# Performance work log

Hardware: AMD Instinct MI355X
Metric: run time of the kernel (lower is better)

The kernel has to match this reference:

```python
import jax, jax.numpy as jnp
import numpy as np

N, E, H = 50000, 300000, 8  # nodes, edges, FeaStConv heads (PyG default)


def _lin_init(k, fan_in, fan_out):
    k1, k2 = jax.random.split(k)
    s = 1.0 / np.sqrt(fan_in)
    w = jax.random.uniform(k1, (fan_in, fan_out), jnp.float32, -s, s)
    b = jax.random.uniform(k2, (fan_out,), jnp.float32, -s, s)
    return w, b


def _conv_init(k, cin, cout):
    k1, k2 = jax.random.split(k)
    w = jax.random.normal(k1, (cin, H * cout), jnp.float32) * 0.1   # weight
    u = jax.random.normal(k2, (cin, H), jnp.float32) * 0.1          # attention u
    c = jnp.zeros((H,), jnp.float32)                                 # attention bias
    b = jnp.zeros((cout,), jnp.float32)                              # output bias
    return w, u, c, b


def setup_inputs() -> dict:
    key = jax.random.key(0)
    ks = jax.random.split(key, 10)
    x = jax.random.normal(ks[0], (N, 3), jnp.float32)
    src = jax.random.randint(ks[1], (E,), 0, N)
    dst = jax.random.randint(ks[2], (E,), 0, N)
    dst = jnp.where(src == dst, (dst + 1) % N, dst)  # no self loops in raw edge list
    edge_index = jnp.stack([src, dst]).astype(jnp.int64)
    labels = (jax.random.uniform(ks[3], (N, 1)) < 0.1).astype(jnp.float32)
    lin1_w, lin1_b = _lin_init(ks[4], 3, 16)
    c1_w, c1_u, c1_c, c1_b = _conv_init(ks[5], 16, 32)
    c2_w, c2_u, c2_c, c2_b = _conv_init(ks[6], 32, 64)
    c3_w, c3_u, c3_c, c3_b = _conv_init(ks[7], 64, 128)
    lin2_w, lin2_b = _lin_init(ks[8], 128, 1024)
    lin3_w, lin3_b = _lin_init(ks[9], 1024, 1)
    return dict(x=x, edge_index=edge_index, labels=labels,
                lin1_w=lin1_w, lin1_b=lin1_b,
                c1_w=c1_w, c1_u=c1_u, c1_c=c1_c, c1_b=c1_b,
                c2_w=c2_w, c2_u=c2_u, c2_c=c2_c, c2_b=c2_b,
                c3_w=c3_w, c3_u=c3_u, c3_c=c3_c, c3_b=c3_b,
                lin2_w=lin2_w, lin2_b=lin2_b, lin3_w=lin3_w, lin3_b=lin3_b)


def feast_conv(x, src, dst, W, u, c, b):
    """PyG FeaStConv: gather x_i/x_j, head-softmax attention on (x_j - x_i),
    per-edge weighted sum over heads, mean-scatter to destination nodes."""
    n = x.shape[0]
    loop = jnp.arange(n, dtype=src.dtype)
    s = jnp.concatenate([src, loop])  # add self loops (PyG default)
    d = jnp.concatenate([dst, loop])
    xi = x[d]
    xj = x[s]
    q = jax.nn.softmax((xj - xi) @ u + c, axis=-1)           # [E+N, H]
    m = (xj @ W).reshape(xj.shape[0], H, -1)                  # [E+N, H, O]
    msg = jnp.einsum('eh,eho->eo', q, m)                      # [E+N, O]
    agg = jax.ops.segment_sum(msg, d, num_segments=n)
    cnt = jax.ops.segment_sum(jnp.ones_like(d, dtype=msg.dtype), d, num_segments=n)
    return agg / cnt[:, None] + b                             # mean aggregation + bias


def reference(x, edge_index, labels,
              lin1_w, lin1_b,
              c1_w, c1_u, c1_c, c1_b,
              c2_w, c2_u, c2_c, c2_b,
              c3_w, c3_u, c3_c, c3_b,
              lin2_w, lin2_b, lin3_w, lin3_b):
    src, dst = edge_index[0], edge_index[1]
    h = jax.nn.relu(x @ lin1_w + lin1_b)
    h = jax.nn.relu(feast_conv(h, src, dst, c1_w, c1_u, c1_c, c1_b))
    h = jax.nn.relu(feast_conv(h, src, dst, c2_w, c2_u, c2_c, c2_b))
    h = jax.nn.relu(feast_conv(h, src, dst, c3_w, c3_u, c3_c, c3_b))
    h = jax.nn.relu(h @ lin2_w + lin2_b)
    p = jax.nn.sigmoid(h @ lin3_w + lin3_b)                   # [N, 1]
    # generate_weights: class-balanced per-element BCE weights
    n = labels.shape[0]
    pos = jnp.sum(labels)
    neg = n - pos
    w = jnp.where(labels == 1, n / (2.0 * pos), n / (2.0 * neg))
    # torch-style BCE with log clamped at -100
    bce = -(labels * jnp.clip(jnp.log(p), -100.0, None)
            + (1.0 - labels) * jnp.clip(jnp.log(1.0 - p), -100.0, None))
    loss = jnp.mean(w * bce)
    return loss, p
```

## Files before the change

### kernel.cpp

```cpp
#include <hip/hip_runtime.h>
#include <math.h>

#define NN 50000
#define NE 300000

typedef short s8v __attribute__((ext_vector_type(8)));
typedef float f4v __attribute__((ext_vector_type(4)));

__device__ inline unsigned short f2bf(float f) {
    union { float f; unsigned int u; } v; v.f = f;
    unsigned int r = v.u + 0x7FFFu + ((v.u >> 16) & 1u);
    return (unsigned short)(r >> 16);
}

__global__ void lin1_kernel(const float* __restrict__ x,
                            const float* __restrict__ w,
                            const float* __restrict__ b,
                            float* __restrict__ out) {
    int idx = blockIdx.x * 256 + threadIdx.x;
    if (idx >= NN * 16) return;
    int n = idx >> 4, o = idx & 15;
    float v = x[n*3+0]*w[o] + x[n*3+1]*w[16+o] + x[n*3+2]*w[32+o] + b[o];
    out[idx] = fmaxf(v, 0.f);
}

template<int CIN>
__global__ void a_kernel(const float* __restrict__ h,
                         const float* __restrict__ u,
                         float* __restrict__ a) {
    int idx = blockIdx.x * 256 + threadIdx.x;
    if (idx >= NN * 8) return;
    int n = idx >> 3, hd = idx & 7;
    float acc = 0.f;
    #pragma unroll
    for (int k = 0; k < CIN; ++k) acc += h[(size_t)n*CIN + k] * u[k*8 + hd];
    a[idx] = acc;
}

__global__ void hist_kernel(const int* __restrict__ dst, int* __restrict__ cnt) {
    int e = blockIdx.x * 256 + threadIdx.x;
    if (e < NE) atomicAdd(&cnt[dst[e]], 1);
}

__global__ void scan1_kernel(const int* __restrict__ cnt, int* __restrict__ rp,
                             int* __restrict__ bpart) {
    __shared__ int sh[256];
    int tid = threadIdx.x;
    int gid = blockIdx.x * 256 + tid;
    int v = (gid < NN) ? cnt[gid] : 0;
    sh[tid] = v;
    __syncthreads();
    for (int off = 1; off < 256; off <<= 1) {
        int t = (tid >= off) ? sh[tid - off] : 0;
        __syncthreads();
        sh[tid] += t;
        __syncthreads();
    }
    if (gid < NN) rp[gid] = sh[tid] - v;
    if (tid == 255) bpart[blockIdx.x] = sh[tid];
}

__global__ void scan2_kernel(int* __restrict__ bpart, int nblk) {
    __shared__ int sh[256];
    int tid = threadIdx.x;
    int v = (tid < nblk) ? bpart[tid] : 0;
    sh[tid] = v;
    __syncthreads();
    for (int off = 1; off < 256; off <<= 1) {
        int t = (tid >= off) ? sh[tid - off] : 0;
        __syncthreads();
        sh[tid] += t;
        __syncthreads();
    }
    bpart[tid] = sh[tid] - v;
}

__global__ void scan3_kernel(int* __restrict__ rp, const int* __restrict__ bpart) {
    int gid = blockIdx.x * 256 + threadIdx.x;
    if (gid < NN) rp[gid] += bpart[blockIdx.x];
    if (gid == 0) rp[NN] = NE;
}

__global__ void scatter_kernel(const int* __restrict__ src, const int* __restrict__ dst,
                               const int* __restrict__ rp, int* __restrict__ fill,
                               int* __restrict__ ssrc, int* __restrict__ sdst) {
    int e = blockIdx.x * 256 + threadIdx.x;
    if (e >= NE) return;
    int d = dst[e];
    int pos = rp[d] + atomicAdd(&fill[d], 1);
    ssrc[pos] = src[e];
    sdst[pos] = d;
}

__global__ void q_sorted_kernel(const int* __restrict__ ssrc,
                                const int* __restrict__ sdst,
                                const float* __restrict__ a,
                                const float* __restrict__ c,
                                float* __restrict__ qs) {
    int j = blockIdx.x * 256 + threadIdx.x;
    if (j >= NE) return;
    int s = ssrc[j], d = sdst[j];
    const float4* as = (const float4*)(a + (size_t)s*8);
    const float4* ad = (const float4*)(a + (size_t)d*8);
    float4 s0 = as[0], s1 = as[1], d0 = ad[0], d1 = ad[1];
    float lg[8] = { s0.x-d0.x+c[0], s0.y-d0.y+c[1], s0.z-d0.z+c[2], s0.w-d0.w+c[3],
                    s1.x-d1.x+c[4], s1.y-d1.y+c[5], s1.z-d1.z+c[6], s1.w-d1.w+c[7] };
    float m = lg[0];
    #pragma unroll
    for (int h = 1; h < 8; ++h) m = fmaxf(m, lg[h]);
    float sum = 0.f;
    #pragma unroll
    for (int h = 0; h < 8; ++h) { lg[h] = __expf(lg[h]-m); sum += lg[h]; }
    float inv = 1.f / sum;
    float4* qp = (float4*)(qs + (size_t)j*8);
    qp[0] = make_float4(lg[0]*inv, lg[1]*inv, lg[2]*inv, lg[3]*inv);
    qp[1] = make_float4(lg[4]*inv, lg[5]*inv, lg[6]*inv, lg[7]*inv);
}

template<int HPER>
__device__ inline void load_qv(const float* __restrict__ qs, int j, int hg, float* qv) {
    if constexpr (HPER == 2) {
        float2 t = *(const float2*)(qs + (size_t)j*8 + hg*2);
        qv[0] = t.x; qv[1] = t.y;
    } else if constexpr (HPER == 4) {
        float4 t = *(const float4*)(qs + (size_t)j*8 + hg*4);
        qv[0] = t.x; qv[1] = t.y; qv[2] = t.z; qv[3] = t.w;
    } else {
        float4 t0 = *(const float4*)(qs + (size_t)j*8);
        float4 t1 = *(const float4*)(qs + (size_t)j*8 + 4);
        qv[0] = t0.x; qv[1] = t0.y; qv[2] = t0.z; qv[3] = t0.w;
        qv[4] = t1.x; qv[5] = t1.y; qv[6] = t1.z; qv[7] = t1.w;
    }
}

template<int CIN>
__global__ __launch_bounds__(256) void agg_kernel(
        const float* __restrict__ hin, const float* __restrict__ cbias,
        const int* __restrict__ rowptr, const int* __restrict__ ssrc,
        const float* __restrict__ qs, unsigned short* __restrict__ g) {
    constexpr int HPER = CIN / 8;
    constexpr int LG = (CIN == 16) ? 4 : (CIN == 32) ? 5 : 6;
    const int lane = threadIdx.x & 63;
    const int d = blockIdx.x * 4 + (threadIdx.x >> 6);
    const int k = lane & (CIN - 1);
    const int hg = lane >> LG;
    float m = cbias[0];
    #pragma unroll
    for (int h = 1; h < 8; ++h) m = fmaxf(m, cbias[h]);
    float ssum = 0.f;
    #pragma unroll
    for (int h = 0; h < 8; ++h) ssum += __expf(cbias[h] - m);
    float sinv = 1.f / ssum;
    float xd = hin[(size_t)d*CIN + k];
    float acc[HPER];
    #pragma unroll
    for (int i = 0; i < HPER; ++i)
        acc[i] = __expf(cbias[hg*HPER + i] - m) * sinv * xd;
    int j0 = rowptr[d], j1 = rowptr[d+1];
    int j = j0;
    for (; j + 2 <= j1; j += 2) {
        int s0 = ssrc[j], s1 = ssrc[j+1];
        float xv0 = hin[(size_t)s0*CIN + k];
        float xv1 = hin[(size_t)s1*CIN + k];
        float qv0[HPER], qv1[HPER];
        load_qv<HPER>(qs, j, hg, qv0);
        load_qv<HPER>(qs, j+1, hg, qv1);
        #pragma unroll
        for (int i = 0; i < HPER; ++i) acc[i] += qv0[i]*xv0 + qv1[i]*xv1;
    }
    if (j < j1) {
        int s0 = ssrc[j];
        float xv0 = hin[(size_t)s0*CIN + k];
        float qv0[HPER];
        load_qv<HPER>(qs, j, hg, qv0);
        #pragma unroll
        for (int i = 0; i < HPER; ++i) acc[i] += qv0[i]*xv0;
    }
    #pragma unroll
    for (int i = 0; i < HPER; ++i)
        g[(size_t)d*(8*CIN) + (hg*HPER + i)*CIN + k] = f2bf(acc[i]);
}

template<int CIN, int O>
__device__ inline void packw_feast_body(const float* __restrict__ W,
                                        unsigned short* __restrict__ wp, int t) {
    constexpr int NS = (8*CIN) / 32;
    int l = t & 63;
    int s = (t >> 6) % NS;
    int ct = t / (64 * NS);
    int c = ct*16 + (l & 15);
    int kk0 = s*32 + (l >> 4) * 8;
    union { unsigned short u[8]; s8v v; } o;
    #pragma unroll
    for (int i = 0; i < 8; ++i) {
        int kk = kk0 + i;
        int h = kk / CIN, k = kk & (CIN - 1);
        o.u[i] = f2bf(W[(size_t)k*(8*O) + h*O + c]);
    }
    *(s8v*)(wp + (size_t)t*8) = o.v;
}

__device__ inline void packw_lin_body(const float* __restrict__ W,
                                      unsigned short* __restrict__ wp, int t) {
    int l = t & 63;
    int s = (t >> 6) & 3;
    int ctg = t >> 8;
    int c = ctg*16 + (l & 15);
    int k0 = s*32 + (l >> 4) * 8;
    union { unsigned short u[8]; s8v v; } o;
    #pragma unroll
    for (int i = 0; i < 8; ++i) o.u[i] = f2bf(W[(size_t)(k0+i)*1024 + c]);
    *(s8v*)(wp + (size_t)t*8) = o.v;
}

__global__ void prep_kernel(const float* __restrict__ l2w, unsigned short* __restrict__ w2p,
                            const float* __restrict__ wf1w, unsigned short* __restrict__ wf1,
                            const float* __restrict__ wf2w, unsigned short* __restrict__ wf2,
                            const float* __restrict__ wf3w, unsigned short* __restrict__ wf3,
                            int* __restrict__ fill, int* __restrict__ fill2,
                            float* __restrict__ z, float* __restrict__ scal) {
    int b = blockIdx.x;
    int tid = threadIdx.x;
    if (b < 64)  { packw_lin_body(l2w, w2p, b*256 + tid); return; }
    b -= 64;
    if (b < 2)   { packw_feast_body<16,32>(wf1w, wf1, b*256 + tid); return; }
    b -= 2;
    if (b < 8)   { packw_feast_body<32,64>(wf2w, wf2, b*256 + tid); return; }
    b -= 8;
    if (b < 32)  { packw_feast_body<64,128>(wf3w, wf3, b*256 + tid); return; }
    b -= 32;
    int idx = b*256 + tid;
    if (idx < NN)            fill[idx] = 0;
    else if (idx < 2*NN)     fill2[idx - NN] = 0;
    else if (idx < 3*NN)     z[idx - 2*NN] = 0.f;
    else if (idx < 3*NN+16)  scal[idx - 3*NN] = 0.f;
}

template<int K, int O, int CH, bool BF16OUT>
__global__ __launch_bounds__(256) void gemm_feast(
        const unsigned short* __restrict__ g, const unsigned short* __restrict__ wp,
        const int* __restrict__ rowptr, const float* __restrict__ b,
        float* __restrict__ houtf, unsigned short* __restrict__ houtb) {
    constexpr int NS = K / 32;
    constexpr int NCT = O / 16;
    __shared__ unsigned short bsh[CH*NS*64*8];
    const int l = threadIdx.x & 63;
    const int w = threadIdx.x >> 6;
    const int base = blockIdx.x * 64 + w * 16;
    int arow = base + (l & 15); if (arow >= NN) arow = NN - 1;
    const int koff = (l >> 4) * 8;
    s8v af[NS];
    #pragma unroll
    for (int s = 0; s < NS; ++s)
        af[s] = *(const s8v*)(g + (size_t)arow*K + s*32 + koff);
    float invc[4];
    #pragma unroll
    for (int r = 0; r < 4; ++r) {
        int n = base + (l >> 4)*4 + r; if (n >= NN) n = NN - 1;
        invc[r] = 1.f / (float)(rowptr[n+1] - rowptr[n] + 1);
    }
    #pragma unroll 1
    for (int ct0 = 0; ct0 < NCT; ct0 += CH) {
        __syncthreads();
        const int4* sp = (const int4*)(wp + (size_t)ct0*NS*512);
        int4* dp = (int4*)bsh;
        #pragma unroll 1
        for (int i = threadIdx.x; i < CH*NS*64; i += 256) dp[i] = sp[i];
        __syncthreads();
        #pragma unroll 1
        for (int cc = 0; cc < CH; ++cc) {
            f4v accA = {0.f,0.f,0.f,0.f}, accB = {0.f,0.f,0.f,0.f};
            #pragma unroll
            for (int s = 0; s < NS/2; ++s) {
                s8v bf = *(const s8v*)(bsh + ((size_t)(cc*NS + s)*64 + l)*8);
                accA = __builtin_amdgcn_mfma_f32_16x16x32_bf16(af[s], bf, accA, 0, 0, 0);
            }
            #pragma unroll
            for (int s = NS/2; s < NS; ++s) {
                s8v bf = *(const s8v*)(bsh + ((size_t)(cc*NS + s)*64 + l)*8);
                accB = __builtin_amdgcn_mfma_f32_16x16x32_bf16(af[s], bf, accB, 0, 0, 0);
            }
            int col = (ct0 + cc)*16 + (l & 15);
            float bb = b[col];
            #pragma unroll
            for (int r = 0; r < 4; ++r) {
                int n = base + (l >> 4)*4 + r;
                float v = fmaxf((accA[r]+accB[r])*invc[r] + bb, 0.f);
                if (n < NN) {
                    if constexpr (BF16OUT) houtb[(size_t)n*O + col] = f2bf(v);
                    else                   houtf[(size_t)n*O + col] = v;
                }
            }
        }
    }
}

__global__ __launch_bounds__(256) void lin23z_kernel(
        const unsigned short* __restrict__ h4b, const unsigned short* __restrict__ w2p,
        const float* __restrict__ b2, const float* __restrict__ w3,
        float* __restrict__ z) {
    const int l = threadIdx.x & 63;
    const int w = threadIdx.x >> 6;
    const int ctg = blockIdx.y;
    const int rowbase = blockIdx.x * 256 + w * 64;
    const int koff = (l >> 4) * 8;
    s8v bf0[4], bf1[4], bf2[4], bf3[4];
    #pragma unroll
    for (int s = 0; s < 4; ++s) {
        bf0[s] = *(const s8v*)(w2p + ((size_t)((ctg*4+0)*4 + s)*64 + l)*8);
        bf1[s] = *(const s8v*)(w2p + ((size_t)((ctg*4+1)*4 + s)*64 + l)*8);
        bf2[s] = *(const s8v*)(w2p + ((size_t)((ctg*4+2)*4 + s)*64 + l)*8);
        bf3[s] = *(const s8v*)(w2p + ((size_t)((ctg*4+3)*4 + s)*64 + l)*8);
    }
    float w3c[4], b2c[4];
    #pragma unroll
    for (int c = 0; c < 4; ++c) {
        int col = (ctg*4 + c)*16 + (l & 15);
        w3c[c] = w3[col]; b2c[c] = b2[col];
    }
    #pragma unroll 1
    for (int t = 0; t < 4; ++t) {
        int base = rowbase + t*16;
        int arow = base + (l & 15); if (arow >= NN) arow = NN - 1;
        s8v af[4];
        #pragma unroll
        for (int s = 0; s < 4; ++s)
            af[s] = *(const s8v*)(h4b + (size_t)arow*128 + s*32 + koff);
        float zp0 = 0.f, zp1 = 0.f, zp2 = 0.f, zp3 = 0.f;
        #pragma unroll
        for (int c = 0; c < 4; ++c) {
            const s8v* bf = (c == 0) ? bf0 : (c == 1) ? bf1 : (c == 2) ? bf2 : bf3;
            f4v accA = {0.f,0.f,0.f,0.f}, accB = {0.f,0.f,0.f,0.f};
            accA = __builtin_amdgcn_mfma_f32_16x16x32_bf16(af[0], bf[0], accA, 0, 0, 0);
            accA = __builtin_amdgcn_mfma_f32_16x16x32_bf16(af[1], bf[1], accA, 0, 0, 0);
            accB = __builtin_amdgcn_mfma_f32_16x16x32_bf16(af[2], bf[2], accB, 0, 0, 0);
            accB = __builtin_amdgcn_mfma_f32_16x16x32_bf16(af[3], bf[3], accB, 0, 0, 0);
            zp0 += fmaxf(accA[0]+accB[0] + b2c[c], 0.f) * w3c[c];
            zp1 += fmaxf(accA[1]+accB[1] + b2c[c], 0.f) * w3c[c];
            zp2 += fmaxf(accA[2]+accB[2] + b2c[c], 0.f) * w3c[c];
            zp3 += fmaxf(accA[3]+accB[3] + b2c[c], 0.f) * w3c[c];
        }
        #pragma unroll
        for (int m = 1; m < 16; m <<= 1) {
            zp0 += __shfl_xor(zp0, m, 64);
            zp1 += __shfl_xor(zp1, m, 64);
            zp2 += __shfl_xor(zp2, m, 64);
            zp3 += __shfl_xor(zp3, m, 64);
        }
        if ((l & 15) == 0) {
            int r0 = base + (l >> 4) * 4;
            if (r0+0 < NN) atomicAdd(&z[r0+0], zp0);
            if (r0+1 < NN) atomicAdd(&z[r0+1], zp1);
            if (r0+2 < NN) atomicAdd(&z[r0+2], zp2);
            if (r0+3 < NN) atomicAdd(&z[r0+3], zp3);
        }
    }
}

__global__ void sigmoid_kernel(const float* __restrict__ z,
                               const float* __restrict__ b3,
                               float* __restrict__ p) {
    int n = blockIdx.x * 256 + threadIdx.x;
    if (n < NN) p[n] = 1.f / (1.f + expf(-(z[n] + b3[0])));
}

__global__ void loss_pass_kernel(const float* __restrict__ labels,
                                 const float* __restrict__ p,
                                 float* __restrict__ scal) {
    __shared__ float sh0[256], sh1[256], sh2[256];
    int tid = threadIdx.x;
    float pos = 0.f, sp = 0.f, sn = 0.f;
    for (int n = blockIdx.x*256 + tid; n < NN; n += gridDim.x*256) {
        float yv = labels[n], pv = p[n];
        if (yv == 1.0f) { pos += 1.f; sp -= fmaxf(logf(pv), -100.f); }
        else            { sn -= fmaxf(logf(1.f - pv), -100.f); }
    }
    sh0[tid] = pos; sh1[tid] = sp; sh2[tid] = sn;
    __syncthreads();
    for (int off = 128; off; off >>= 1) {
        if (tid < off) {
            sh0[tid] += sh0[tid+off];
            sh1[tid] += sh1[tid+off];
            sh2[tid] += sh2[tid+off];
        }
        __syncthreads();
    }
    if (tid == 0) {
        atomicAdd(&scal[0], sh0[0]);
        atomicAdd(&scal[1], sh1[0]);
        atomicAdd(&scal[2], sh2[0]);
    }
}

__global__ void loss_final_kernel(const float* __restrict__ scal,
                                  float* __restrict__ out) {
    float pos = scal[0];
    out[0] = scal[1] / (2.f*pos) + scal[2] / (2.f*((float)NN - pos));
}

extern "C" void kernel_launch(void* const* d_in, const int* in_sizes, int n_in,
                              void* d_out, int out_size, void* d_ws, size_t ws_size,
                              hipStream_t stream) {
    (void)in_sizes; (void)n_in; (void)out_size; (void)ws_size;
    const float* x   = (const float*)d_in[0];
    const int*   ei  = (const int*)d_in[1];
    const float* labels = (const float*)d_in[2];
    const float* l1w = (const float*)d_in[3];
    const float* l1b = (const float*)d_in[4];
    const float* cw[3] = {(const float*)d_in[5], (const float*)d_in[9],  (const float*)d_in[13]};
    const float* cu[3] = {(const float*)d_in[6], (const float*)d_in[10], (const float*)d_in[14]};
    const float* cc[3] = {(const float*)d_in[7], (const float*)d_in[11], (const float*)d_in[15]};
    const float* cb[3] = {(const float*)d_in[8], (const float*)d_in[12], (const float*)d_in[16]};
    const float* l2w = (const float*)d_in[17];
    const float* l2b = (const float*)d_in[18];
    const float* l3w = (const float*)d_in[19];
    const float* l3b = (const float*)d_in[20];
    const int* srcp = ei;
    const int* dstp = ei + NE;
    float* out = (float*)d_out;

    float* ws = (float*)d_ws;
    size_t off = 0;
    auto alloc = [&](size_t n) { float* p = ws + off; off += (n + 15) & ~(size_t)15; return p; };
    float* hA = alloc((size_t)NN*64);
    float* hB = alloc((size_t)NN*128);
    float* a  = alloc((size_t)NN*8);
    unsigned short* g   = (unsigned short*)alloc((size_t)NN*256);
    unsigned short* w2p = (unsigned short*)alloc(65536);
    unsigned short* wf1 = (unsigned short*)alloc(2048);
    unsigned short* wf2 = (unsigned short*)alloc(8192);
    unsigned short* wf3 = (unsigned short*)alloc(32768);
    float* z    = alloc(NN);
    float* scal = alloc(16);
    int* rowptr = (int*)alloc(50016);
    int* fill   = (int*)alloc(NN);
    int* fill2  = (int*)alloc(NN);
    int* ssrc   = (int*)alloc(NE);
    int* sdst   = (int*)alloc(NE);
    int* bpart  = (int*)alloc(256);
    float* qs1 = hB;
    float* qs2 = hA;
    float* qs3 = hB;
    unsigned short* h4b = (unsigned short*)hB;

    const int SCAN_BLKS = (NN + 255) / 256;
    const int GB = (NN + 63) / 64;
    const int PREP_BLKS = 106 + (3*NN + 16 + 255) / 256;

    prep_kernel<<<PREP_BLKS, 256, 0, stream>>>(l2w, w2p, cw[0], wf1, cw[1], wf2,
                                               cw[2], wf3, fill, fill2, z, scal);
    hist_kernel<<<(NE+255)/256, 256, 0, stream>>>(dstp, fill);
    scan1_kernel<<<SCAN_BLKS, 256, 0, stream>>>(fill, rowptr, bpart);
    scan2_kernel<<<1, 256, 0, stream>>>(bpart, SCAN_BLKS);
    scan3_kernel<<<SCAN_BLKS, 256, 0, stream>>>(rowptr, bpart);
    scatter_kernel<<<(NE+255)/256, 256, 0, stream>>>(srcp, dstp, rowptr, fill2, ssrc, sdst);

    lin1_kernel<<<(NN*16+255)/256, 256, 0, stream>>>(x, l1w, l1b, hA);

    a_kernel<16><<<(NN*8+255)/256, 256, 0, stream>>>(hA, cu[0], a);
    q_sorted_kernel<<<(NE+255)/256, 256, 0, stream>>>(ssrc, sdst, a, cc[0], qs1);
    agg_kernel<16><<<NN/4, 256, 0, stream>>>(hA, cc[0], rowptr, ssrc, qs1, g);
    gemm_feast<128,32,2,false><<<GB, 256, 0, stream>>>(g, wf1, rowptr, cb[0], hB, nullptr);

    a_kernel<32><<<(NN*8+255)/256, 256, 0, stream>>>(hB, cu[1], a);
    q_sorted_kernel<<<(NE+255)/256, 256, 0, stream>>>(ssrc, sdst, a, cc[1], qs2);
    agg_kernel<32><<<NN/4, 256, 0, stream>>>(hB, cc[1], rowptr, ssrc, qs2, g);
    gemm_feast<256,64,4,false><<<GB, 256, 0, stream>>>(g, wf2, rowptr, cb[1], hA, nullptr);

    a_kernel<64><<<(NN*8+255)/256, 256, 0, stream>>>(hA, cu[2], a);
    q_sorted_kernel<<<(NE+255)/256, 256, 0, stream>>>(ssrc, sdst, a, cc[2], qs3);
    agg_kernel<64><<<NN/4, 256, 0, stream>>>(hA, cc[2], rowptr, ssrc, qs3, g);
    gemm_feast<512,128,2,true><<<GB, 256, 0, stream>>>(g, wf3, rowptr, cb[2], nullptr, h4b);

    lin23z_kernel<<<dim3((NN+255)/256, 16), 256, 0, stream>>>(h4b, w2p, l2b, l3w, z);
    sigmoid_kernel<<<SCAN_BLKS, 256, 0, stream>>>(z, l3b, out + 1);

    loss_pass_kernel<<<256, 256, 0, stream>>>(labels, out + 1, scal);
    loss_final_kernel<<<1, 1, 0, stream>>>(scal, out);
}
```

Baseline: 271.2 us.

## Fuse lin1, attention logits, scan stages and loss tail into neighbouring kernels

Folds lin1 and the first attention projection into the prep kernel. The next layer's per-node attention logits are now computed in the GEMM epilogue with a shuffle reduction, which removes the a_kernel launches and re-reading h. The two-pass block-offset scan is merged into one scanfix kernel that reduces preceding partials per block. Sigmoid, loss pass and the final scalar are merged into one kernel that uses a last-block atomic counter. This cuts about seven launches and some memory traffic, at the cost of more registers in the GEMM epilogue and redundant partial sums in the scan.

```diff
diff --git a/kernel.cpp b/kernel.cpp
--- a/kernel.cpp
+++ b/kernel.cpp
@@ -13,28 +13,83 @@
     return (unsigned short)(r >> 16);
 }
 
-__global__ void lin1_kernel(const float* __restrict__ x,
-                            const float* __restrict__ w,
-                            const float* __restrict__ b,
-                            float* __restrict__ out) {
-    int idx = blockIdx.x * 256 + threadIdx.x;
-    if (idx >= NN * 16) return;
-    int n = idx >> 4, o = idx & 15;
-    float v = x[n*3+0]*w[o] + x[n*3+1]*w[16+o] + x[n*3+2]*w[32+o] + b[o];
-    out[idx] = fmaxf(v, 0.f);
-}
-
-template<int CIN>
-__global__ void a_kernel(const float* __restrict__ h,
-                         const float* __restrict__ u,
-                         float* __restrict__ a) {
-    int idx = blockIdx.x * 256 + threadIdx.x;
-    if (idx >= NN * 8) return;
-    int n = idx >> 3, hd = idx & 7;
-    float acc = 0.f;
-    #pragma unroll
-    for (int k = 0; k < CIN; ++k) acc += h[(size_t)n*CIN + k] * u[k*8 + hd];
-    a[idx] = acc;
+template<int CIN, int O>
+__device__ inline void packw_feast_body(const float* __restrict__ W,
+                                        unsigned short* __restrict__ wp, int t) {
+    constexpr int NS = (8*CIN) / 32;
+    int l = t & 63;
+    int s = (t >> 6) % NS;
+    int ct = t / (64 * NS);
+    int c = ct*16 + (l & 15);
+    int kk0 = s*32 + (l >> 4) * 8;
+    union { unsigned short u[8]; s8v v; } o;
+    #pragma unroll
+    for (int i = 0; i < 8; ++i) {
+        int kk = kk0 + i;
+        int h = kk / CIN, k = kk & (CIN - 1);
+        o.u[i] = f2bf(W[(size_t)k*(8*O) + h*O + c]);
+    }
+    *(s8v*)(wp + (size_t)t*8) = o.v;
+}
+
+__device__ inline void packw_lin_body(const float* __restrict__ W,
+                                      unsigned short* __restrict__ wp, int t) {
+    int l = t & 63;
+    int s = (t >> 6) & 3;
+    int ctg = t >> 8;
+    int c = ctg*16 + (l & 15);
+    int k0 = s*32 + (l >> 4) * 8;
+    union { unsigned short u[8]; s8v v; } o;
+    #pragma unroll
+    for (int i = 0; i < 8; ++i) o.u[i] = f2bf(W[(size_t)(k0+i)*1024 + c]);
+    *(s8v*)(wp + (size_t)t*8) = o.v;
+}
+
+__global__ __launch_bounds__(256) void prep_kernel(
+        const float* __restrict__ l2w, unsigned short* __restrict__ w2p,
+        const float* __restrict__ wf1w, unsigned short* __restrict__ wf1,
+        const float* __restrict__ wf2w, unsigned short* __restrict__ wf2,
+        const float* __restrict__ wf3w, unsigned short* __restrict__ wf3,
+        int* __restrict__ fill, int* __restrict__ fill2,
+        float* __restrict__ z, float* __restrict__ scal,
+        const float* __restrict__ x, const float* __restrict__ l1w,
+        const float* __restrict__ l1b, const float* __restrict__ u1,
+        float* __restrict__ h1, float* __restrict__ a) {
+    __shared__ float hsh[16][16];
+    int b = blockIdx.x;
+    int tid = threadIdx.x;
+    if (b < 64)  { packw_lin_body(l2w, w2p, b*256 + tid); return; }
+    b -= 64;
+    if (b < 2)   { packw_feast_body<16,32>(wf1w, wf1, b*256 + tid); return; }
+    b -= 2;
+    if (b < 8)   { packw_feast_body<32,64>(wf2w, wf2, b*256 + tid); return; }
+    b -= 8;
+    if (b < 32)  { packw_feast_body<64,128>(wf3w, wf3, b*256 + tid); return; }
+    b -= 32;
+    if (b < 587) {
+        int idx = b*256 + tid;
+        if (idx < NN)            fill[idx] = 0;
+        else if (idx < 2*NN)     fill2[idx - NN] = 0;
+        else if (idx < 3*NN)     z[idx - 2*NN] = 0.f;
+        else if (idx < 3*NN+16)  scal[idx - 3*NN] = 0.f;
+        return;
+    }
+    b -= 587;
+    int n0 = b * 16;
+    int node = n0 + (tid >> 4), col = tid & 15;
+    float v = x[node*3+0]*l1w[col] + x[node*3+1]*l1w[16+col]
+            + x[node*3+2]*l1w[32+col] + l1b[col];
+    v = fmaxf(v, 0.f);
+    h1[(size_t)node*16 + col] = v;
+    hsh[tid >> 4][col] = v;
+    __syncthreads();
+    if (tid < 128) {
+        int t2 = tid >> 3, h = tid & 7;
+        float acc = 0.f;
+        #pragma unroll
+        for (int k = 0; k < 16; ++k) acc += hsh[t2][k] * u1[k*8 + h];
+        a[(size_t)(n0 + t2)*8 + h] = acc;
+    }
 }
 
 __global__ void hist_kernel(const int* __restrict__ dst, int* __restrict__ cnt) {
@@ -60,24 +115,20 @@
     if (tid == 255) bpart[blockIdx.x] = sh[tid];
 }
 
-__global__ void scan2_kernel(int* __restrict__ bpart, int nblk) {
+__global__ void scanfix_kernel(int* __restrict__ rp, const int* __restrict__ bpart,
+                               int nblk) {
     __shared__ int sh[256];
     int tid = threadIdx.x;
-    int v = (tid < nblk) ? bpart[tid] : 0;
-    sh[tid] = v;
+    int bx = blockIdx.x;
+    sh[tid] = (tid < bx && tid < nblk) ? bpart[tid] : 0;
     __syncthreads();
-    for (int off = 1; off < 256; off <<= 1) {
-        int t = (tid >= off) ? sh[tid - off] : 0;
+    for (int off = 128; off; off >>= 1) {
+        if (tid < off) sh[tid] += sh[tid + off];
         __syncthreads();
-        sh[tid] += t;
-        __syncthreads();
-    }
-    bpart[tid] = sh[tid] - v;
-}
-
-__global__ void scan3_kernel(int* __restrict__ rp, const int* __restrict__ bpart) {
-    int gid = blockIdx.x * 256 + threadIdx.x;
-    if (gid < NN) rp[gid] += bpart[blockIdx.x];
+    }
+    int add = sh[0];
+    int gid = bx * 256 + tid;
+    if (gid < NN) rp[gid] += add;
     if (gid == 0) rp[NN] = NE;
 }
 
@@ -181,66 +232,12 @@
         g[(size_t)d*(8*CIN) + (hg*HPER + i)*CIN + k] = f2bf(acc[i]);
 }
 
-template<int CIN, int O>
-__device__ inline void packw_feast_body(const float* __restrict__ W,
-                                        unsigned short* __restrict__ wp, int t) {
-    constexpr int NS = (8*CIN) / 32;
-    int l = t & 63;
-    int s = (t >> 6) % NS;
-    int ct = t / (64 * NS);
-    int c = ct*16 + (l & 15);
-    int kk0 = s*32 + (l >> 4) * 8;
-    union { unsigned short u[8]; s8v v; } o;
-    #pragma unroll
-    for (int i = 0; i < 8; ++i) {
-        int kk = kk0 + i;
-        int h = kk / CIN, k = kk & (CIN - 1);
-        o.u[i] = f2bf(W[(size_t)k*(8*O) + h*O + c]);
-    }
-    *(s8v*)(wp + (size_t)t*8) = o.v;
-}
-
-__device__ inline void packw_lin_body(const float* __restrict__ W,
-                                      unsigned short* __restrict__ wp, int t) {
-    int l = t & 63;
-    int s = (t >> 6) & 3;
-    int ctg = t >> 8;
-    int c = ctg*16 + (l & 15);
-    int k0 = s*32 + (l >> 4) * 8;
-    union { unsigned short u[8]; s8v v; } o;
-    #pragma unroll
-    for (int i = 0; i < 8; ++i) o.u[i] = f2bf(W[(size_t)(k0+i)*1024 + c]);
-    *(s8v*)(wp + (size_t)t*8) = o.v;
-}
-
-__global__ void prep_kernel(const float* __restrict__ l2w, unsigned short* __restrict__ w2p,
-                            const float* __restrict__ wf1w, unsigned short* __restrict__ wf1,
-                            const float* __restrict__ wf2w, unsigned short* __restrict__ wf2,
-                            const float* __restrict__ wf3w, unsigned short* __restrict__ wf3,
-                            int* __restrict__ fill, int* __restrict__ fill2,
-                            float* __restrict__ z, float* __restrict__ scal) {
-    int b = blockIdx.x;
-    int tid = threadIdx.x;
-    if (b < 64)  { packw_lin_body(l2w, w2p, b*256 + tid); return; }
-    b -= 64;
-    if (b < 2)   { packw_feast_body<16,32>(wf1w, wf1, b*256 + tid); return; }
-    b -= 2;
-    if (b < 8)   { packw_feast_body<32,64>(wf2w, wf2, b*256 + tid); return; }
-    b -= 8;
-    if (b < 32)  { packw_feast_body<64,128>(wf3w, wf3, b*256 + tid); return; }
-    b -= 32;
-    int idx = b*256 + tid;
-    if (idx < NN)            fill[idx] = 0;
-    else if (idx < 2*NN)     fill2[idx - NN] = 0;
-    else if (idx < 3*NN)     z[idx - 2*NN] = 0.f;
-    else if (idx < 3*NN+16)  scal[idx - 3*NN] = 0.f;
-}
-
-template<int K, int O, int CH, bool BF16OUT>
+template<int K, int O, int CH, bool BF16OUT, bool AEPI>
 __global__ __launch_bounds__(256) void gemm_feast(
         const unsigned short* __restrict__ g, const unsigned short* __restrict__ wp,
         const int* __restrict__ rowptr, const float* __restrict__ b,
-        float* __restrict__ houtf, unsigned short* __restrict__ houtb) {
+        float* __restrict__ houtf, unsigned short* __restrict__ houtb,
+        const float* __restrict__ unext, float* __restrict__ aout) {
     constexpr int NS = K / 32;
     constexpr int NCT = O / 16;
     __shared__ unsigned short bsh[CH*NS*64*8];
@@ -258,6 +255,13 @@
     for (int r = 0; r < 4; ++r) {
         int n = base + (l >> 4)*4 + r; if (n >= NN) n = NN - 1;
         invc[r] = 1.f / (float)(rowptr[n+1] - rowptr[n] + 1);
+    }
+    float apart[4][8];
+    if constexpr (AEPI) {
+        #pragma unroll
+        for (int r = 0; r < 4; ++r)
+            #pragma unroll
+            for (int h = 0; h < 8; ++h) apart[r][h] = 0.f;
     }
     #pragma unroll 1
     for (int ct0 = 0; ct0 < NCT; ct0 += CH) {
@@ -282,16 +286,41 @@
             }
             int col = (ct0 + cc)*16 + (l & 15);
             float bb = b[col];
+            float uv[8];
+            if constexpr (AEPI) {
+                #pragma unroll
+                for (int h = 0; h < 8; ++h) uv[h] = unext[col*8 + h];
+            }
             #pragma unroll
             for (int r = 0; r < 4; ++r) {
                 int n = base + (l >> 4)*4 + r;
                 float v = fmaxf((accA[r]+accB[r])*invc[r] + bb, 0.f);
+                if constexpr (AEPI) {
+                    #pragma unroll
+                    for (int h = 0; h < 8; ++h) apart[r][h] += v * uv[h];
+                }
                 if (n < NN) {
                     if constexpr (BF16OUT) houtb[(size_t)n*O + col] = f2bf(v);
                     else                   houtf[(size_t)n*O + col] = v;
                 }
             }
         }
+    }
+    if constexpr (AEPI) {
+        #pragma unroll
+        for (int r = 0; r < 4; ++r)
+            #pragma unroll
+            for (int h = 0; h < 8; ++h) {
+                float v = apart[r][h];
+                v += __shfl_xor(v, 1, 64);
+                v += __shfl_xor(v, 2, 64);
+                v += __shfl_xor(v, 4, 64);
+                v += __shfl_xor(v, 8, 64);
+                if ((l & 15) == 0) {
+                    int n = base + (l >> 4)*4 + r;
+                    if (n < NN) aout[(size_t)n*8 + h] = v;
+                }
+            }
     }
 }
 
@@ -357,23 +386,22 @@
     }
 }
 
-__global__ void sigmoid_kernel(const float* __restrict__ z,
-                               const float* __restrict__ b3,
-                               float* __restrict__ p) {
-    int n = blockIdx.x * 256 + threadIdx.x;
-    if (n < NN) p[n] = 1.f / (1.f + expf(-(z[n] + b3[0])));
-}
-
-__global__ void loss_pass_kernel(const float* __restrict__ labels,
-                                 const float* __restrict__ p,
-                                 float* __restrict__ scal) {
+__global__ void finish_kernel(const float* __restrict__ labels,
+                              const float* __restrict__ z,
+                              const float* __restrict__ b3,
+                              float* __restrict__ p,
+                              float* __restrict__ scal,
+                              float* __restrict__ out, int nblk) {
     __shared__ float sh0[256], sh1[256], sh2[256];
     int tid = threadIdx.x;
+    int n = blockIdx.x * 256 + tid;
     float pos = 0.f, sp = 0.f, sn = 0.f;
-    for (int n = blockIdx.x*256 + tid; n < NN; n += gridDim.x*256) {
-        float yv = labels[n], pv = p[n];
-        if (yv == 1.0f) { pos += 1.f; sp -= fmaxf(logf(pv), -100.f); }
-        else            { sn -= fmaxf(logf(1.f - pv), -100.f); }
+    if (n < NN) {
+        float pv = 1.f / (1.f + expf(-(z[n] + b3[0])));
+        p[n] = pv;
+        float yv = labels[n];
+        if (yv == 1.0f) { pos = 1.f; sp = -fmaxf(logf(pv), -100.f); }
+        else            { sn = -fmaxf(logf(1.f - pv), -100.f); }
     }
     sh0[tid] = pos; sh1[tid] = sp; sh2[tid] = sn;
     __syncthreads();
@@ -389,13 +417,15 @@
         atomicAdd(&scal[0], sh0[0]);
         atomicAdd(&scal[1], sh1[0]);
         atomicAdd(&scal[2], sh2[0]);
-    }
-}
-
-__global__ void loss_final_kernel(const float* __restrict__ scal,
-                                  float* __restrict__ out) {
-    float pos = scal[0];
-    out[0] = scal[1] / (2.f*pos) + scal[2] / (2.f*((float)NN - pos));
+        __threadfence();
+        int t = atomicAdd((int*)&scal[4], 1);
+        if (t == nblk - 1) {
+            float posT = atomicAdd(&scal[0], 0.f);
+            float spT  = atomicAdd(&scal[1], 0.f);
+            float snT  = atomicAdd(&scal[2], 0.f);
+            out[0] = spT / (2.f*posT) + snT / (2.f*((float)NN - posT));
+        }
+    }
 }
 
 extern "C" void kernel_launch(void* const* d_in, const int* in_sizes, int n_in,
@@ -445,36 +475,28 @@
 
     const int SCAN_BLKS = (NN + 255) / 256;
     const int GB = (NN + 63) / 64;
-    const int PREP_BLKS = 106 + (3*NN + 16 + 255) / 256;
+    const int PREP_BLKS = 106 + 587 + NN/16;
 
     prep_kernel<<<PREP_BLKS, 256, 0, stream>>>(l2w, w2p, cw[0], wf1, cw[1], wf2,
-                                               cw[2], wf3, fill, fill2, z, scal);
+                                               cw[2], wf3, fill, fill2, z, scal,
+                                               x, l1w, l1b, cu[0], hA, a);
     hist_kernel<<<(NE+255)/256, 256, 0, stream>>>(dstp, fill);
     scan1_kernel<<<SCAN_BLKS, 256, 0, stream>>>(fill, rowptr, bpart);
-    scan2_kernel<<<1, 256, 0, stream>>>(bpart, SCAN_BLKS);
-    scan3_kernel<<<SCAN_BLKS, 256, 0, stream>>>(rowptr, bpart);
+    scanfix_kernel<<<SCAN_BLKS, 256, 0, stream>>>(rowptr, bpart, SCAN_BLKS);
     scatter_kernel<<<(NE+255)/256, 256, 0, stream>>>(srcp, dstp, rowptr, fill2, ssrc, sdst);
 
-    lin1_kernel<<<(NN*16+255)/256, 256, 0, stream>>>(x, l1w, l1b, hA);
-
-    a_kernel<16><<<(NN*8+255)/256, 256, 0, stream>>>(hA, cu[0], a);
     q_sorted_kernel<<<(NE+255)/256, 256, 0, stream>>>(ssrc, sdst, a, cc[0], qs1);
     agg_kernel<16><<<NN/4, 256, 0, stream>>>(hA, cc[0], rowptr, ssrc, qs1, g);
-    gemm_feast<128,32,2,false><<<GB, 256, 0, stream>>>(g, wf1, rowptr, cb[0], hB, nullptr);
-
-    a_kernel<32><<<(NN*8+255)/256, 256, 0, stream>>>(hB, cu[1], a);
+    gemm_feast<128,32,2,false,true><<<GB, 256, 0, stream>>>(g, wf1, rowptr, cb[0], hB, nullptr, cu[1], a);
+
     q_sorted_kernel<<<(NE+255)/256, 256, 0, stream>>>(ssrc, sdst, a, cc[1], qs2);
     agg_kernel<32><<<NN/4, 256, 0, stream>>>(hB, cc[1], rowptr, ssrc, qs2, g);
-    gemm_feast<256,64,4,false><<<GB, 256, 0, stream>>>(g, wf2, rowptr, cb[1], hA, nullptr);
-
-    a_kernel<64><<<(NN*8+255)/256, 256, 0, stream>>>(hA, cu[2], a);
+    gemm_feast<256,64,4,false,true><<<GB, 256, 0, stream>>>(g, wf2, rowptr, cb[1], hA, nullptr, cu[2], a);
+
     q_sorted_kernel<<<(NE+255)/256, 256, 0, stream>>>(ssrc, sdst, a, cc[2], qs3);
     agg_kernel<64><<<NN/4, 256, 0, stream>>>(hA, cc[2], rowptr, ssrc, qs3, g);
-    gemm_feast<512,128,2,true><<<GB, 256, 0, stream>>>(g, wf3, rowptr, cb[2], nullptr, h4b);
+    gemm_feast<512,128,2,true,false><<<GB, 256, 0, stream>>>(g, wf3, rowptr, cb[2], nullptr, h4b, nullptr, nullptr);
 
     lin23z_kernel<<<dim3((NN+255)/256, 16), 256, 0, stream>>>(h4b, w2p, l2b, l3w, z);
-    sigmoid_kernel<<<SCAN_BLKS, 256, 0, stream>>>(z, l3b, out + 1);
-
-    loss_pass_kernel<<<256, 256, 0, stream>>>(labels, out + 1, scal);
-    loss_final_kernel<<<1, 1, 0, stream>>>(scal, out);
-}
+    finish_kernel<<<SCAN_BLKS, 256, 0, stream>>>(labels, z, l3b, out + 1, scal, out, SCAN_BLKS);
+}
```

Measured after the change: 259.4 us. 4.4% less time.
